# Kernel tuning notes

Hardware: AMD Instinct MI355X
Metric: run time of the kernel (lower is better)

## Reference

```python
import jax, jax.numpy as jnp
import numpy as np

N, E, IN, HID, H, OUT, G = 20000, 320000, 128, 64, 6, 10, 64
NEG_SLOPE = 0.2


def gat_conv(x, W, a_src, a_dst, b, src, dst):
    # x: [N, F_in]; W: [F_in, H*C]; a_src/a_dst: [H, C]; b: [H*C]
    n = x.shape[0]
    h = (x @ W).reshape(n, H, HID)                      # [N, H, C]
    alpha_s = jnp.einsum('nhc,hc->nh', h, a_src)        # [N, H]
    alpha_d = jnp.einsum('nhc,hc->nh', h, a_dst)
    e = jax.nn.leaky_relu(alpha_s[src] + alpha_d[dst], NEG_SLOPE)  # [E, H]
    # segment softmax over incoming edges of each destination node
    m = jax.ops.segment_max(e, dst, num_segments=n)
    ex = jnp.exp(e - m[dst])
    s = jax.ops.segment_sum(ex, dst, num_segments=n)
    alpha = ex / (s[dst] + 1e-16)                       # [E, H]
    out = jax.ops.segment_sum(alpha[:, :, None] * h[src], dst, num_segments=n)
    return out.reshape(n, H * HID) + b


def setup_inputs() -> dict:
    key = jax.random.key(0)
    ks = jax.random.split(key, 24)
    p = lambda k, shp: jax.random.normal(k, shp, dtype=jnp.float32) * 0.1
    inp = {
        'x': jax.random.normal(ks[0], (N, IN), dtype=jnp.float32),
        'edge_index': jax.random.randint(ks[1], (2, E), 0, N),
        'batch': jnp.sort(jax.random.randint(ks[2], (N,), 0, G)),
        'W1': p(ks[3], (IN, H * HID)), 'a1_src': p(ks[4], (H, HID)), 'a1_dst': p(ks[5], (H, HID)), 'b1': p(ks[6], (H * HID,)),
        'W2': p(ks[7], (H * HID, H * HID)), 'a2_src': p(ks[8], (H, HID)), 'a2_dst': p(ks[9], (H, HID)), 'b2': p(ks[10], (H * HID,)),
        'Ws1': p(ks[11], (IN, H * HID)), 'as1_src': p(ks[12], (H, HID)), 'as1_dst': p(ks[13], (H, HID)), 'bs1': p(ks[14], (H * HID,)),
        'Ws2': p(ks[15], (H * HID, H * HID)), 'as2_src': p(ks[16], (H, HID)), 'as2_dst': p(ks[17], (H, HID)), 'bs2': p(ks[18], (H * HID,)),
        'r1_w': p(ks[19], (H * HID, HID)), 'r1_b': p(ks[20], (HID,)),
        'r2_w': p(ks[21], (HID, OUT)), 'r2_b': p(ks[22], (OUT,)),
    }
    return inp


def reference(x, edge_index, batch, W1, a1_src, a1_dst, b1, W2, a2_src, a2_dst, b2,
              Ws1, as1_src, as1_dst, bs1, Ws2, as2_src, as2_dst, bs2,
              r1_w, r1_b, r2_w, r2_b):
    # PyG GATConv adds self-loops by default
    loop = jnp.arange(N, dtype=edge_index.dtype)
    src = jnp.concatenate([edge_index[0], loop])
    dst = jnp.concatenate([edge_index[1], loop])

    # skip branch (dropout = identity in eval)
    xs = jax.nn.relu(gat_conv(x, Ws1, as1_src, as1_dst, bs1, src, dst))
    xs = jax.nn.relu(gat_conv(xs, Ws2, as2_src, as2_dst, bs2, src, dst))

    # main branch
    h = jax.nn.relu(gat_conv(x, W1, a1_src, a1_dst, b1, src, dst))
    h = jax.nn.relu(gat_conv(h, W2, a2_src, a2_dst, b2, src, dst))

    h = h + xs

    # global mean pool over graphs
    sums = jax.ops.segment_sum(h, batch, num_segments=G)          # [G, H*C]
    cnts = jax.ops.segment_sum(jnp.ones((N,), h.dtype), batch, num_segments=G)
    x_readout = sums / jnp.maximum(cnts, 1.0)[:, None]

    x_global = jax.nn.relu(x_readout @ r1_w + r1_b) @ r2_w + r2_b  # [G, OUT]
    return (jnp.squeeze(x_global), x_readout)
```

## Files before the change

### kernel.cpp

```cpp
#include <hip/hip_runtime.h>
#include <hip/hip_fp16.h>

#define NN 20000
#define EE 320000
#define ETOT 340000
#define FIN 128
#define NH 6
#define FF 384
#define NOUT 10
#define NG 64
#define NEG 0.2f
#define PCH 32
#define NB ((NN + 255) / 256)

typedef short short8 __attribute__((ext_vector_type(8)));
typedef float f32x4 __attribute__((ext_vector_type(4)));

__device__ __half g_h16[(size_t)NN * FF];
__device__ float g_bufB[(size_t)NN * FF];
__device__ float g_bufC[(size_t)NN * FF];
__device__ unsigned short g_featHi[(size_t)NN * FF];
__device__ unsigned short g_featLo[(size_t)NN * FF];
__device__ unsigned short g_xHi[(size_t)NN * FIN];
__device__ unsigned short g_xLo[(size_t)NN * FIN];
__device__ unsigned short g_WtHi[4][FF * FF];
__device__ float g_alS[4][NN * NH];
__device__ float g_alD[4][NN * NH];
__device__ int g_rowptr[NN + 1];
__device__ int g_cnt[NN];
__device__ int g_cur[NN];
__device__ int g_blocksum[NB];
__device__ int g_colsrc[ETOT];
__device__ float g_pool[NG * FF];
__device__ int g_gcnt[NG];

__device__ __forceinline__ unsigned short f2bf(float f) {
  unsigned u = __float_as_uint(f);
  u += 0x7FFFu + ((u >> 16) & 1u);
  return (unsigned short)(u >> 16);
}
__device__ __forceinline__ float bf2f(unsigned short s) {
  return __uint_as_float(((unsigned)s) << 16);
}

__device__ __forceinline__ void gl_lds16(const void* g, void* l) {
  __builtin_amdgcn_global_load_lds(
      (const __attribute__((address_space(1))) unsigned int*)(unsigned long long)g,
      (__attribute__((address_space(3))) unsigned int*)(unsigned int)(unsigned long long)l,
      16, 0, 0);
}

__device__ __forceinline__ void mfma_acc(f32x4& c, short8 a, short8 b) {
  asm("v_mfma_f32_16x16x32_bf16 %0, %1, %2, %0" : "+v"(c) : "v"(a), "v"(b));
}

__device__ __forceinline__ void fmix(float2& acc, unsigned hv, float w) {
  asm("v_fma_mix_f32 %0, %2, %3, %0 op_sel:[0,0,0] op_sel_hi:[1,0,0]\n\t"
      "v_fma_mix_f32 %1, %2, %3, %1 op_sel:[1,0,0] op_sel_hi:[1,0,0]"
      : "+v"(acc.x), "+v"(acc.y)
      : "v"(hv), "v"(w));
}

__global__ __launch_bounds__(256) void k_wprep(const float* __restrict__ W, int K, int widx) {
  int i = blockIdx.x * 256 + threadIdx.x;
  if (i >= K * FF) return;
  int k = i / FF, c = i % FF;
  g_WtHi[widx][c * K + k] = f2bf(W[i]);
}

__global__ __launch_bounds__(256) void k_zero() {
  int i = blockIdx.x * 256 + threadIdx.x;
  if (i < NN) g_cnt[i] = 0;
  if (i < NG * FF) g_pool[i] = 0.f;
  if (i < NG) g_gcnt[i] = 0;
  if (i < 4 * NN * NH) {
    (&g_alS[0][0])[i] = 0.f;
    (&g_alD[0][0])[i] = 0.f;
  }
}

__global__ __launch_bounds__(256) void k_hist(const int* __restrict__ ei) {
  int i = blockIdx.x * 256 + threadIdx.x;
  if (i >= ETOT) return;
  int d = (i < EE) ? ei[EE + i] : (i - EE);
  atomicAdd(&g_cnt[d], 1);
}

__global__ __launch_bounds__(256) void k_scan_blk() {
  int b = blockIdx.x;
  int tid = threadIdx.x;
  int i = b * 256 + tid;
  int lane = tid & 63, wid = tid >> 6;
  int v = (i < NN) ? g_cnt[i] : 0;
  int s = v;
  #pragma unroll
  for (int off = 1; off < 64; off <<= 1) {
    int t = __shfl_up(s, off);
    if (lane >= off) s += t;
  }
  __shared__ int wsum[4];
  if (lane == 63) wsum[wid] = s;
  __syncthreads();
  int woff = 0;
  #pragma unroll
  for (int w = 0; w < 4; ++w) woff += (w < wid) ? wsum[w] : 0;
  if (i < NN) g_rowptr[i] = woff + s - v;
  if (tid == 0) g_blocksum[b] = wsum[0] + wsum[1] + wsum[2] + wsum[3];
}

__global__ __launch_bounds__(128) void k_scan_top() {
  int tid = threadIdx.x;
  int lane = tid & 63, wid = tid >> 6;
  int v = (tid < NB) ? g_blocksum[tid] : 0;
  int s = v;
  #pragma unroll
  for (int off = 1; off < 64; off <<= 1) {
    int t = __shfl_up(s, off);
    if (lane >= off) s += t;
  }
  __shared__ int wsum[2];
  if (lane == 63) wsum[wid] = s;
  __syncthreads();
  int woff = (wid == 1) ? wsum[0] : 0;
  int excl = woff + s - v;
  if (tid < NB) g_blocksum[tid] = excl;
  if (tid == NB - 1) g_rowptr[NN] = excl + v;
}

__global__ __launch_bounds__(256) void k_scan_add() {
  int i = blockIdx.x * 256 + threadIdx.x;
  if (i >= NN) return;
  int r = g_rowptr[i] + g_blocksum[blockIdx.x];
  g_rowptr[i] = r;
  g_cur[i] = r;
}

__global__ __launch_bounds__(256) void k_scatter(const int* __restrict__ ei) {
  int i = blockIdx.x * 256 + threadIdx.x;
  if (i >= ETOT) return;
  int s, d;
  if (i < EE) { s = ei[i]; d = ei[EE + i]; } else { s = d = i - EE; }
  int pos = atomicAdd(&g_cur[d], 1);
  g_colsrc[pos] = s;
}

__global__ __launch_bounds__(256) void k_split(const float* __restrict__ xin) {
  int n4 = (NN * FIN) >> 2;
  const float4* s4 = (const float4*)xin;
  ushort4* oh4 = (ushort4*)g_xHi;
  ushort4* ol4 = (ushort4*)g_xLo;
  for (int i = blockIdx.x * blockDim.x + threadIdx.x; i < n4; i += gridDim.x * blockDim.x) {
    float4 v = s4[i];
    ushort4 h, l;
    h.x = f2bf(v.x); l.x = f2bf(v.x - bf2f(h.x));
    h.y = f2bf(v.y); l.y = f2bf(v.y - bf2f(h.y));
    h.z = f2bf(v.z); l.z = f2bf(v.z - bf2f(h.z));
    h.w = f2bf(v.w); l.w = f2bf(v.w - bf2f(h.w));
    oh4[i] = h; ol4[i] = l;
  }
}

__global__ __launch_bounds__(256) void k_gemm(int asel, int widx, int K, int layer,
                                              const float* __restrict__ asr,
                                              const float* __restrict__ adt) {
  __shared__ unsigned short lA[128 * 64];
  __shared__ unsigned short lB[128 * 64];
  const unsigned short* Ah = asel ? g_featHi : g_xHi;
  const unsigned short* Al = asel ? g_featLo : g_xLo;
  const unsigned short* Bh = g_WtHi[widx];
  const int m0 = blockIdx.x * 128;
  const int n0 = blockIdx.y * 128;
  const int tid = threadIdx.x;
  const int wave = tid >> 6, lane = tid & 63;
  const int wm = wave >> 1, wn = wave & 1;
  const int srow = lane >> 3;
  const int scol = (lane & 7) * 8;

  f32x4 acc[4][4] = {};

  for (int t = 0; t < 2; ++t) {
    const unsigned short* Ap = t ? Al : Ah;
    for (int k0 = 0; k0 < K; k0 += 64) {
      __syncthreads();
      #pragma unroll
      for (int it = 0; it < 4; ++it) {
        int c = wave * 4 + it;
        int rA = c * 8 + srow;
        int gr = m0 + rA; gr = (gr < NN) ? gr : (NN - 1);
        gl_lds16(Ap + (size_t)gr * K + k0 + scol, (unsigned short*)lA + c * 512);
        int cB = n0 + rA;
        gl_lds16(Bh + (size_t)cB * K + k0 + scol, (unsigned short*)lB + c * 512);
      }
      __syncthreads();
      #pragma unroll
      for (int kk = 0; kk < 64; kk += 32) {
        const int kb = kk + (lane >> 4) * 8;
        const int r16 = lane & 15;
        short8 af[4], bfr[4];
        #pragma unroll
        for (int mf = 0; mf < 4; ++mf)
          af[mf] = *(const short8*)&lA[(wm * 64 + mf * 16 + r16) * 64 + kb];
        #pragma unroll
        for (int nf = 0; nf < 4; ++nf)
          bfr[nf] = *(const short8*)&lB[(wn * 64 + nf * 16 + r16) * 64 + kb];
        #pragma unroll
        for (int mf = 0; mf < 4; ++mf)
          #pragma unroll
          for (int nf = 0; nf < 4; ++nf)
            mfma_acc(acc[mf][nf], af[mf], bfr[nf]);
      }
    }
  }
  asm volatile("s_nop 7\n\ts_nop 7" :::);

  const int r16 = lane & 15;
  #pragma unroll
  for (int mf = 0; mf < 4; ++mf) {
    #pragma unroll
    for (int nf = 0; nf < 4; ++nf) {
      int col = n0 + wn * 64 + nf * 16 + r16;
      int rb = m0 + wm * 64 + mf * 16 + ((lane >> 4) << 2);
      #pragma unroll
      for (int j = 0; j < 4; ++j) {
        int r = rb + j;
        if (r < NN) g_h16[(size_t)r * FF + col] = __float2half(acc[mf][nf][j]);
      }
    }
  }
  const int hd = blockIdx.y * 2 + wn;
  float as_v[4], ad_v[4];
  #pragma unroll
  for (int nf = 0; nf < 4; ++nf) {
    as_v[nf] = asr[hd * 64 + nf * 16 + r16];
    ad_v[nf] = adt[hd * 64 + nf * 16 + r16];
  }
  float* alS = g_alS[layer];
  float* alD = g_alD[layer];
  #pragma unroll
  for (int mf = 0; mf < 4; ++mf) {
    #pragma unroll
    for (int j = 0; j < 4; ++j) {
      float ps = 0.f, pd = 0.f;
      #pragma unroll
      for (int nf = 0; nf < 4; ++nf) {
        ps = fmaf(acc[mf][nf][j], as_v[nf], ps);
        pd = fmaf(acc[mf][nf][j], ad_v[nf], pd);
      }
      #pragma unroll
      for (int off = 1; off < 16; off <<= 1) {
        ps += __shfl_xor(ps, off);
        pd += __shfl_xor(pd, off);
      }
      int r = m0 + wm * 64 + mf * 16 + ((lane >> 4) << 2) + j;
      if (r16 == 0 && r < NN) {
        atomicAdd(&alS[r * NH + hd], ps);
        atomicAdd(&alD[r * NH + hd], pd);
      }
    }
  }
}

__global__ __launch_bounds__(256) void k_edge(const float* __restrict__ bias, int mode, int layer) {
  __shared__ int l_se[4][64];
  __shared__ float l_wf[4][NH][64];
  int wv = threadIdx.x >> 6;
  int node = blockIdx.x * 4 + wv;
  int lane = threadIdx.x & 63;
  if (node >= NN) return;
  const float* aS = g_alS[layer];
  const float* aD = g_alD[layer];
  const int lo = g_rowptr[node], hi = g_rowptr[node + 1];
  const int deg = hi - lo;
  float ad[NH];
  #pragma unroll
  for (int h = 0; h < NH; ++h) ad[h] = aD[node * NH + h];

  const bool hiHalf = (lane >= 32);
  float m[NH], inv[NH];
  const bool fast = (deg <= 64);

  if (fast) {
    bool val = lane < deg;
    int s = val ? g_colsrc[lo + lane] : 0;
    const float2* ap = (const float2*)(aS + (size_t)s * NH);
    float2 p0 = ap[0], p1 = ap[1], p2 = ap[2];
    float v[NH] = {p0.x + ad[0], p0.y + ad[1], p1.x + ad[2],
                   p1.y + ad[3], p2.x + ad[4], p2.y + ad[5]};
    float mm[NH], w[NH], ss[NH];
    #pragma unroll
    for (int h = 0; h < NH; ++h) {
      v[h] = (v[h] > 0.f) ? v[h] : NEG * v[h];
      mm[h] = val ? v[h] : -1e30f;
    }
    #pragma unroll
    for (int h = 0; h < NH; ++h)
      #pragma unroll
      for (int off = 32; off > 0; off >>= 1)
        mm[h] = fmaxf(mm[h], __shfl_xor(mm[h], off));
    #pragma unroll
    for (int h = 0; h < NH; ++h) {
      w[h] = val ? __expf(v[h] - mm[h]) : 0.f;
      ss[h] = w[h];
    }
    #pragma unroll
    for (int h = 0; h < NH; ++h)
      #pragma unroll
      for (int off = 32; off > 0; off >>= 1)
        ss[h] += __shfl_xor(ss[h], off);
    l_se[wv][lane] = s;
    #pragma unroll
    for (int h = 0; h < NH; ++h)
      l_wf[wv][h][lane] = w[h] * __frcp_rn(ss[h] + 1e-16f);
  } else {
    #pragma unroll
    for (int h = 0; h < NH; ++h) m[h] = -1e30f;
    for (int e = lo + lane; e < hi; e += 64) {
      int se = g_colsrc[e];
      #pragma unroll
      for (int h = 0; h < NH; ++h) {
        float v = aS[se * NH + h] + ad[h];
        v = (v > 0.f) ? v : NEG * v;
        m[h] = fmaxf(m[h], v);
      }
    }
    #pragma unroll
    for (int h = 0; h < NH; ++h)
      #pragma unroll
      for (int off = 32; off > 0; off >>= 1)
        m[h] = fmaxf(m[h], __shfl_xor(m[h], off));
    float ss[NH] = {0.f, 0.f, 0.f, 0.f, 0.f, 0.f};
    for (int e = lo + lane; e < hi; e += 64) {
      int se = g_colsrc[e];
      #pragma unroll
      for (int h = 0; h < NH; ++h) {
        float v = aS[se * NH + h] + ad[h];
        v = (v > 0.f) ? v : NEG * v;
        ss[h] += __expf(v - m[h]);
      }
    }
    #pragma unroll
    for (int h = 0; h < NH; ++h) {
      #pragma unroll
      for (int off = 32; off > 0; off >>= 1)
        ss[h] += __shfl_xor(ss[h], off);
      inv[h] = __frcp_rn(ss[h] + 1e-16f);
    }
  }

  float2 accA[3] = {{0.f,0.f},{0.f,0.f},{0.f,0.f}};
  float2 accB[3] = {{0.f,0.f},{0.f,0.f},{0.f,0.f}};
  float2 accC[3] = {{0.f,0.f},{0.f,0.f},{0.f,0.f}};
  float2 accD[3] = {{0.f,0.f},{0.f,0.f},{0.f,0.f}};

  if (fast) {
    const int h0 = hiHalf ? 1 : 0, h1 = hiHalf ? 3 : 2, h2 = hiHalf ? 5 : 4;
    int e = 0;
    for (; e + 3 < deg; e += 4) {
      int4 se4 = *(int4*)&l_se[wv][e];
      float4 w0 = *(float4*)&l_wf[wv][h0][e];
      float4 w1 = *(float4*)&l_wf[wv][h1][e];
      float4 w2 = *(float4*)&l_wf[wv][h2][e];
      const unsigned* r0 = (const unsigned*)(g_h16 + (size_t)se4.x * FF) + lane;
      const unsigned* r1 = (const unsigned*)(g_h16 + (size_t)se4.y * FF) + lane;
      const unsigned* r2 = (const unsigned*)(g_h16 + (size_t)se4.z * FF) + lane;
      const unsigned* r3 = (const unsigned*)(g_h16 + (size_t)se4.w * FF) + lane;
      unsigned ha[3] = {r0[0], r0[64], r0[128]};
      unsigned hb[3] = {r1[0], r1[64], r1[128]};
      unsigned hc[3] = {r2[0], r2[64], r2[128]};
      unsigned hd[3] = {r3[0], r3[64], r3[128]};
      fmix(accA[0], ha[0], w0.x); fmix(accB[0], hb[0], w0.y);
      fmix(accC[0], hc[0], w0.z); fmix(accD[0], hd[0], w0.w);
      fmix(accA[1], ha[1], w1.x); fmix(accB[1], hb[1], w1.y);
      fmix(accC[1], hc[1], w1.z); fmix(accD[1], hd[1], w1.w);
      fmix(accA[2], ha[2], w2.x); fmix(accB[2], hb[2], w2.y);
      fmix(accC[2], hc[2], w2.z); fmix(accD[2], hd[2], w2.w);
    }
    for (; e < deg; ++e) {
      int se = l_se[wv][e];
      float wa0 = l_wf[wv][h0][e], wa1 = l_wf[wv][h1][e], wa2 = l_wf[wv][h2][e];
      const unsigned* r0 = (const unsigned*)(g_h16 + (size_t)se * FF) + lane;
      fmix(accA[0], r0[0], wa0);
      fmix(accA[1], r0[64], wa1);
      fmix(accA[2], r0[128], wa2);
    }
  } else {
    for (int e = 0; e < deg; ++e) {
      int se = g_colsrc[lo + e];
      const float* as = aS + (size_t)se * NH;
      float we[NH];
      #pragma unroll
      for (int h = 0; h < NH; ++h) {
        float v = as[h] + ad[h];
        v = (v > 0.f) ? v : NEG * v;
        we[h] = __expf(v - m[h]) * inv[h];
      }
      float wa[3] = {hiHalf ? we[1] : we[0], hiHalf ? we[3] : we[2],
                     hiHalf ? we[5] : we[4]};
      const unsigned* r0 = (const unsigned*)(g_h16 + (size_t)se * FF) + lane;
      unsigned h0v[3] = {r0[0], r0[64], r0[128]};
      #pragma unroll
      for (int c = 0; c < 3; ++c) fmix(accA[c], h0v[c], wa[c]);
    }
  }

  #pragma unroll
  for (int c = 0; c < 3; ++c) {
    float2 bv = *(const float2*)(bias + c * 128 + lane * 2);
    float ox = fmaxf(accA[c].x + accB[c].x + accC[c].x + accD[c].x + bv.x, 0.f);
    float oy = fmaxf(accA[c].y + accB[c].y + accC[c].y + accD[c].y + bv.y, 0.f);
    size_t off = (size_t)node * FF + c * 128 + lane * 2;
    if (mode == 2) {
      unsigned short hx = f2bf(ox), hy = f2bf(oy);
      ushort2 hh = {hx, hy};
      ushort2 ll = {f2bf(ox - bf2f(hx)), f2bf(oy - bf2f(hy))};
      *(ushort2*)(g_featHi + off) = hh;
      *(ushort2*)(g_featLo + off) = ll;
    } else {
      float* out = mode ? g_bufC : g_bufB;
      float2 o = {ox, oy};
      *(float2*)(out + off) = o;
    }
  }
}

__global__ __launch_bounds__(384) void k_pool_acc(const int* __restrict__ batch) {
  int n0 = blockIdx.x * PCH;
  if (n0 >= NN) return;
  int n1 = n0 + PCH; if (n1 > NN) n1 = NN;
  int d = threadIdx.x;
  int cur = batch[n0];
  float acc = 0.f;
  int cnt = 0;
  for (int n = n0; n < n1; ++n) {
    int g = batch[n];
    if (g != cur) {
      atomicAdd(&g_pool[cur * FF + d], acc);
      if (d == 0) atomicAdd(&g_gcnt[cur], cnt);
      acc = 0.f; cnt = 0; cur = g;
    }
    acc += g_bufB[(size_t)n * FF + d] + g_bufC[(size_t)n * FF + d];
    ++cnt;
  }
  atomicAdd(&g_pool[cur * FF + d], acc);
  if (d == 0) atomicAdd(&g_gcnt[cur], cnt);
}

__global__ __launch_bounds__(384) void k_finish(const float* __restrict__ r1w,
                                                const float* __restrict__ r1b,
                                                const float* __restrict__ r2w,
                                                const float* __restrict__ r2b,
                                                float* __restrict__ dout) {
  int g = blockIdx.x;
  int d = threadIdx.x;
  __shared__ float xr[FF];
  __shared__ float hid[64];
  int cnt = g_gcnt[g];
  float denom = (cnt > 0) ? (float)cnt : 1.f;
  float v = g_pool[g * FF + d] / denom;
  xr[d] = v;
  dout[NG * NOUT + g * FF + d] = v;
  __syncthreads();
  if (d < 64) {
    float acc = r1b[d];
    for (int k = 0; k < FF; ++k) acc = fmaf(xr[k], r1w[k * 64 + d], acc);
    hid[d] = fmaxf(acc, 0.f);
  }
  __syncthreads();
  if (d < NOUT) {
    float o = r2b[d];
    #pragma unroll
    for (int j = 0; j < 64; ++j) o = fmaf(hid[j], r2w[j * NOUT + d], o);
    dout[g * NOUT + d] = o;
  }
}

extern "C" void kernel_launch(void* const* d_in, const int* in_sizes, int n_in,
                              void* d_out, int out_size, void* d_ws, size_t ws_size,
                              hipStream_t stream) {
  const float* x    = (const float*)d_in[0];
  const int* ei     = (const int*)d_in[1];
  const int* batch  = (const int*)d_in[2];
  const float* W1   = (const float*)d_in[3];
  const float* a1s  = (const float*)d_in[4];
  const float* a1d  = (const float*)d_in[5];
  const float* b1   = (const float*)d_in[6];
  const float* W2   = (const float*)d_in[7];
  const float* a2s  = (const float*)d_in[8];
  const float* a2d  = (const float*)d_in[9];
  const float* b2   = (const float*)d_in[10];
  const float* Ws1  = (const float*)d_in[11];
  const float* as1s = (const float*)d_in[12];
  const float* as1d = (const float*)d_in[13];
  const float* bs1  = (const float*)d_in[14];
  const float* Ws2  = (const float*)d_in[15];
  const float* as2s = (const float*)d_in[16];
  const float* as2d = (const float*)d_in[17];
  const float* bs2  = (const float*)d_in[18];
  const float* r1w  = (const float*)d_in[19];
  const float* r1b  = (const float*)d_in[20];
  const float* r2w  = (const float*)d_in[21];
  const float* r2b  = (const float*)d_in[22];
  float* out = (float*)d_out;

  dim3 b256(256);
  k_wprep<<<dim3((FIN * FF + 255) / 256), b256, 0, stream>>>(Ws1, FIN, 0);
  k_wprep<<<dim3((FF * FF + 255) / 256), b256, 0, stream>>>(Ws2, FF, 1);
  k_wprep<<<dim3((FIN * FF + 255) / 256), b256, 0, stream>>>(W1, FIN, 2);
  k_wprep<<<dim3((FF * FF + 255) / 256), b256, 0, stream>>>(W2, FF, 3);
  k_zero<<<dim3((4 * NN * NH + 255) / 256), b256, 0, stream>>>();
  k_hist<<<dim3((ETOT + 255) / 256), b256, 0, stream>>>(ei);
  k_scan_blk<<<dim3(NB), b256, 0, stream>>>();
  k_scan_top<<<dim3(1), dim3(128), 0, stream>>>();
  k_scan_add<<<dim3(NB), b256, 0, stream>>>();
  k_scatter<<<dim3((ETOT + 255) / 256), b256, 0, stream>>>(ei);
  k_split<<<dim3(2048), b256, 0, stream>>>(x);

  dim3 gemmGrid((NN + 127) / 128, FF / 128);
  dim3 nodeGrid((NN + 3) / 4);

  k_gemm<<<gemmGrid, b256, 0, stream>>>(0, 0, FIN, 0, as1s, as1d);
  k_edge<<<nodeGrid, b256, 0, stream>>>(bs1, 2, 0);
  k_gemm<<<gemmGrid, b256, 0, stream>>>(1, 1, FF, 1, as2s, as2d);
  k_edge<<<nodeGrid, b256, 0, stream>>>(bs2, 1, 1);
  k_gemm<<<gemmGrid, b256, 0, stream>>>(0, 2, FIN, 2, a1s, a1d);
  k_edge<<<nodeGrid, b256, 0, stream>>>(b1, 2, 2);
  k_gemm<<<gemmGrid, b256, 0, stream>>>(1, 3, FF, 3, a2s, a2d);
  k_edge<<<nodeGrid, b256, 0, stream>>>(b2, 0, 3);
  k_pool_acc<<<dim3((NN + PCH - 1) / PCH), dim3(384), 0, stream>>>(batch);
  k_finish<<<dim3(NG), dim3(384), 0, stream>>>(r1w, r1b, r2w, r2b, out);
}
```

Baseline: 384.3 us.

## Split GAT edge aggregation across heads, one head per block

The edge kernel now launches eight blocks per group of four nodes. Each of the first six handles a single attention head and the last two exit immediately. Each lane computes one head's softmax and gathers a single fp16 value per edge instead of three packed pairs. The aim is more parallelism and lower register pressure per wave. In exchange, row-pointer, index and attention-score reads and the softmax are repeated for every head, gathers become 2-byte loads, and a quarter of the blocks do no work.

```diff
diff --git a/kernel.cpp b/kernel.cpp
--- a/kernel.cpp
+++ b/kernel.cpp
@@ -12,6 +12,7 @@
 #define NEG 0.2f
 #define PCH 32
 #define NB ((NN + 255) / 256)
+#define NBLK ((NN + 3) / 4)
 
 typedef short short8 __attribute__((ext_vector_type(8)));
 typedef float f32x4 __attribute__((ext_vector_type(4)));
@@ -54,13 +55,6 @@
   asm("v_mfma_f32_16x16x32_bf16 %0, %1, %2, %0" : "+v"(c) : "v"(a), "v"(b));
 }
 
-__device__ __forceinline__ void fmix(float2& acc, unsigned hv, float w) {
-  asm("v_fma_mix_f32 %0, %2, %3, %0 op_sel:[0,0,0] op_sel_hi:[1,0,0]\n\t"
-      "v_fma_mix_f32 %1, %2, %3, %1 op_sel:[1,0,0] op_sel_hi:[1,0,0]"
-      : "+v"(acc.x), "+v"(acc.y)
-      : "v"(hv), "v"(w));
-}
-
 __global__ __launch_bounds__(256) void k_wprep(const float* __restrict__ W, int K, int widx) {
   int i = blockIdx.x * 256 + threadIdx.x;
   if (i >= K * FF) return;
@@ -262,164 +256,99 @@
 
 __global__ __launch_bounds__(256) void k_edge(const float* __restrict__ bias, int mode, int layer) {
   __shared__ int l_se[4][64];
-  __shared__ float l_wf[4][NH][64];
+  __shared__ float l_w[4][64];
+  const int chunk = blockIdx.x & 7;
+  if (chunk >= NH) return;
+  const int h = chunk;
   int wv = threadIdx.x >> 6;
-  int node = blockIdx.x * 4 + wv;
+  int node = (blockIdx.x >> 3) * 4 + wv;
   int lane = threadIdx.x & 63;
   if (node >= NN) return;
   const float* aS = g_alS[layer];
   const float* aD = g_alD[layer];
   const int lo = g_rowptr[node], hi = g_rowptr[node + 1];
   const int deg = hi - lo;
-  float ad[NH];
-  #pragma unroll
-  for (int h = 0; h < NH; ++h) ad[h] = aD[node * NH + h];
-
-  const bool hiHalf = (lane >= 32);
-  float m[NH], inv[NH];
+  const float ad = aD[node * NH + h];
   const bool fast = (deg <= 64);
+  float m, inv;
 
   if (fast) {
     bool val = lane < deg;
     int s = val ? g_colsrc[lo + lane] : 0;
-    const float2* ap = (const float2*)(aS + (size_t)s * NH);
-    float2 p0 = ap[0], p1 = ap[1], p2 = ap[2];
-    float v[NH] = {p0.x + ad[0], p0.y + ad[1], p1.x + ad[2],
-                   p1.y + ad[3], p2.x + ad[4], p2.y + ad[5]};
-    float mm[NH], w[NH], ss[NH];
-    #pragma unroll
-    for (int h = 0; h < NH; ++h) {
-      v[h] = (v[h] > 0.f) ? v[h] : NEG * v[h];
-      mm[h] = val ? v[h] : -1e30f;
-    }
-    #pragma unroll
-    for (int h = 0; h < NH; ++h)
-      #pragma unroll
-      for (int off = 32; off > 0; off >>= 1)
-        mm[h] = fmaxf(mm[h], __shfl_xor(mm[h], off));
-    #pragma unroll
-    for (int h = 0; h < NH; ++h) {
-      w[h] = val ? __expf(v[h] - mm[h]) : 0.f;
-      ss[h] = w[h];
-    }
-    #pragma unroll
-    for (int h = 0; h < NH; ++h)
-      #pragma unroll
-      for (int off = 32; off > 0; off >>= 1)
-        ss[h] += __shfl_xor(ss[h], off);
+    float v = aS[s * NH + h] + ad;
+    v = (v > 0.f) ? v : NEG * v;
+    float mm = val ? v : -1e30f;
+    #pragma unroll
+    for (int off = 32; off > 0; off >>= 1)
+      mm = fmaxf(mm, __shfl_xor(mm, off));
+    float w = val ? __expf(v - mm) : 0.f;
+    float ss = w;
+    #pragma unroll
+    for (int off = 32; off > 0; off >>= 1)
+      ss += __shfl_xor(ss, off);
     l_se[wv][lane] = s;
-    #pragma unroll
-    for (int h = 0; h < NH; ++h)
-      l_wf[wv][h][lane] = w[h] * __frcp_rn(ss[h] + 1e-16f);
+    l_w[wv][lane] = w * __frcp_rn(ss + 1e-16f);
   } else {
-    #pragma unroll
-    for (int h = 0; h < NH; ++h) m[h] = -1e30f;
+    m = -1e30f;
     for (int e = lo + lane; e < hi; e += 64) {
       int se = g_colsrc[e];
-      #pragma unroll
-      for (int h = 0; h < NH; ++h) {
-        float v = aS[se * NH + h] + ad[h];
-        v = (v > 0.f) ? v : NEG * v;
-        m[h] = fmaxf(m[h], v);
-      }
-    }
-    #pragma unroll
-    for (int h = 0; h < NH; ++h)
-      #pragma unroll
-      for (int off = 32; off > 0; off >>= 1)
-        m[h] = fmaxf(m[h], __shfl_xor(m[h], off));
-    float ss[NH] = {0.f, 0.f, 0.f, 0.f, 0.f, 0.f};
+      float v = aS[se * NH + h] + ad;
+      v = (v > 0.f) ? v : NEG * v;
+      m = fmaxf(m, v);
+    }
+    #pragma unroll
+    for (int off = 32; off > 0; off >>= 1)
+      m = fmaxf(m, __shfl_xor(m, off));
+    float ss = 0.f;
     for (int e = lo + lane; e < hi; e += 64) {
       int se = g_colsrc[e];
-      #pragma unroll
-      for (int h = 0; h < NH; ++h) {
-        float v = aS[se * NH + h] + ad[h];
-        v = (v > 0.f) ? v : NEG * v;
-        ss[h] += __expf(v - m[h]);
-      }
-    }
-    #pragma unroll
-    for (int h = 0; h < NH; ++h) {
-      #pragma unroll
-      for (int off = 32; off > 0; off >>= 1)
-        ss[h] += __shfl_xor(ss[h], off);
-      inv[h] = __frcp_rn(ss[h] + 1e-16f);
-    }
-  }
-
-  float2 accA[3] = {{0.f,0.f},{0.f,0.f},{0.f,0.f}};
-  float2 accB[3] = {{0.f,0.f},{0.f,0.f},{0.f,0.f}};
-  float2 accC[3] = {{0.f,0.f},{0.f,0.f},{0.f,0.f}};
-  float2 accD[3] = {{0.f,0.f},{0.f,0.f},{0.f,0.f}};
+      float v = aS[se * NH + h] + ad;
+      v = (v > 0.f) ? v : NEG * v;
+      ss += __expf(v - m);
+    }
+    #pragma unroll
+    for (int off = 32; off > 0; off >>= 1)
+      ss += __shfl_xor(ss, off);
+    inv = __frcp_rn(ss + 1e-16f);
+  }
+
+  const unsigned short* tbl = (const unsigned short*)g_h16 + h * 64 + lane;
+  float acc0 = 0.f, acc1 = 0.f, acc2 = 0.f, acc3 = 0.f;
 
   if (fast) {
-    const int h0 = hiHalf ? 1 : 0, h1 = hiHalf ? 3 : 2, h2 = hiHalf ? 5 : 4;
-    int e = 0;
-    for (; e + 3 < deg; e += 4) {
-      int4 se4 = *(int4*)&l_se[wv][e];
-      float4 w0 = *(float4*)&l_wf[wv][h0][e];
-      float4 w1 = *(float4*)&l_wf[wv][h1][e];
-      float4 w2 = *(float4*)&l_wf[wv][h2][e];
-      const unsigned* r0 = (const unsigned*)(g_h16 + (size_t)se4.x * FF) + lane;
-      const unsigned* r1 = (const unsigned*)(g_h16 + (size_t)se4.y * FF) + lane;
-      const unsigned* r2 = (const unsigned*)(g_h16 + (size_t)se4.z * FF) + lane;
-      const unsigned* r3 = (const unsigned*)(g_h16 + (size_t)se4.w * FF) + lane;
-      unsigned ha[3] = {r0[0], r0[64], r0[128]};
-      unsigned hb[3] = {r1[0], r1[64], r1[128]};
-      unsigned hc[3] = {r2[0], r2[64], r2[128]};
-      unsigned hd[3] = {r3[0], r3[64], r3[128]};
-      fmix(accA[0], ha[0], w0.x); fmix(accB[0], hb[0], w0.y);
-      fmix(accC[0], hc[0], w0.z); fmix(accD[0], hd[0], w0.w);
-      fmix(accA[1], ha[1], w1.x); fmix(accB[1], hb[1], w1.y);
-      fmix(accC[1], hc[1], w1.z); fmix(accD[1], hd[1], w1.w);
-      fmix(accA[2], ha[2], w2.x); fmix(accB[2], hb[2], w2.y);
-      fmix(accC[2], hc[2], w2.z); fmix(accD[2], hd[2], w2.w);
-    }
-    for (; e < deg; ++e) {
-      int se = l_se[wv][e];
-      float wa0 = l_wf[wv][h0][e], wa1 = l_wf[wv][h1][e], wa2 = l_wf[wv][h2][e];
-      const unsigned* r0 = (const unsigned*)(g_h16 + (size_t)se * FF) + lane;
-      fmix(accA[0], r0[0], wa0);
-      fmix(accA[1], r0[64], wa1);
-      fmix(accA[2], r0[128], wa2);
+    const int degR = (deg + 3) & ~3;
+    for (int e = 0; e < degR; e += 4) {
+      int4 s4 = *(int4*)&l_se[wv][e];
+      float4 w4 = *(float4*)&l_w[wv][e];
+      float v0 = __half2float(*(const __half*)(tbl + (size_t)s4.x * FF));
+      float v1 = __half2float(*(const __half*)(tbl + (size_t)s4.y * FF));
+      float v2 = __half2float(*(const __half*)(tbl + (size_t)s4.z * FF));
+      float v3 = __half2float(*(const __half*)(tbl + (size_t)s4.w * FF));
+      acc0 = fmaf(w4.x, v0, acc0);
+      acc1 = fmaf(w4.y, v1, acc1);
+      acc2 = fmaf(w4.z, v2, acc2);
+      acc3 = fmaf(w4.w, v3, acc3);
     }
   } else {
-    for (int e = 0; e < deg; ++e) {
-      int se = g_colsrc[lo + e];
-      const float* as = aS + (size_t)se * NH;
-      float we[NH];
-      #pragma unroll
-      for (int h = 0; h < NH; ++h) {
-        float v = as[h] + ad[h];
-        v = (v > 0.f) ? v : NEG * v;
-        we[h] = __expf(v - m[h]) * inv[h];
-      }
-      float wa[3] = {hiHalf ? we[1] : we[0], hiHalf ? we[3] : we[2],
-                     hiHalf ? we[5] : we[4]};
-      const unsigned* r0 = (const unsigned*)(g_h16 + (size_t)se * FF) + lane;
-      unsigned h0v[3] = {r0[0], r0[64], r0[128]};
-      #pragma unroll
-      for (int c = 0; c < 3; ++c) fmix(accA[c], h0v[c], wa[c]);
-    }
-  }
-
-  #pragma unroll
-  for (int c = 0; c < 3; ++c) {
-    float2 bv = *(const float2*)(bias + c * 128 + lane * 2);
-    float ox = fmaxf(accA[c].x + accB[c].x + accC[c].x + accD[c].x + bv.x, 0.f);
-    float oy = fmaxf(accA[c].y + accB[c].y + accC[c].y + accD[c].y + bv.y, 0.f);
-    size_t off = (size_t)node * FF + c * 128 + lane * 2;
-    if (mode == 2) {
-      unsigned short hx = f2bf(ox), hy = f2bf(oy);
-      ushort2 hh = {hx, hy};
-      ushort2 ll = {f2bf(ox - bf2f(hx)), f2bf(oy - bf2f(hy))};
-      *(ushort2*)(g_featHi + off) = hh;
-      *(ushort2*)(g_featLo + off) = ll;
-    } else {
-      float* out = mode ? g_bufC : g_bufB;
-      float2 o = {ox, oy};
-      *(float2*)(out + off) = o;
-    }
+    for (int e = lo; e < hi; ++e) {
+      int se = g_colsrc[e];
+      float v = aS[se * NH + h] + ad;
+      v = (v > 0.f) ? v : NEG * v;
+      float w = __expf(v - m) * inv;
+      acc0 = fmaf(w, __half2float(*(const __half*)(tbl + (size_t)se * FF)), acc0);
+    }
+  }
+
+  float o = acc0 + acc1 + acc2 + acc3 + bias[h * 64 + lane];
+  o = fmaxf(o, 0.f);
+  size_t off = (size_t)node * FF + h * 64 + lane;
+  if (mode == 2) {
+    unsigned short hx = f2bf(o);
+    g_featHi[off] = hx;
+    g_featLo[off] = f2bf(o - bf2f(hx));
+  } else {
+    float* out = mode ? g_bufC : g_bufB;
+    out[off] = o;
   }
 }
 
@@ -516,16 +445,16 @@
   k_split<<<dim3(2048), b256, 0, stream>>>(x);
 
   dim3 gemmGrid((NN + 127) / 128, FF / 128);
-  dim3 nodeGrid((NN + 3) / 4);
+  dim3 edgeGrid(8 * NBLK);
 
   k_gemm<<<gemmGrid, b256, 0, stream>>>(0, 0, FIN, 0, as1s, as1d);
-  k_edge<<<nodeGrid, b256, 0, stream>>>(bs1, 2, 0);
+  k_edge<<<edgeGrid, b256, 0, stream>>>(bs1, 2, 0);
   k_gemm<<<gemmGrid, b256, 0, stream>>>(1, 1, FF, 1, as2s, as2d);
-  k_edge<<<nodeGrid, b256, 0, stream>>>(bs2, 1, 1);
+  k_edge<<<edgeGrid, b256, 0, stream>>>(bs2, 1, 1);
   k_gemm<<<gemmGrid, b256, 0, stream>>>(0, 2, FIN, 2, a1s, a1d);
-  k_edge<<<nodeGrid, b256, 0, stream>>>(b1, 2, 2);
+  k_edge<<<edgeGrid, b256, 0, stream>>>(b1, 2, 2);
   k_gemm<<<gemmGrid, b256, 0, stream>>>(1, 3, FF, 3, a2s, a2d);
-  k_edge<<<nodeGrid, b256, 0, stream>>>(b2, 0, 3);
+  k_edge<<<edgeGrid, b256, 0, stream>>>(b2, 0, 3);
   k_pool_acc<<<dim3((NN + PCH - 1) / PCH), dim3(384), 0, stream>>>(batch);
   k_finish<<<dim3(NG), dim3(384), 0, stream>>>(r1w, r1b, r2w, r2b, out);
 }
```

After: 524.0 us. +36.3%, slower.
